# Kernel tuning notes

Measured on AMD Instinct MI355X. Metric: run time of the kernel, lower is better.

## Reference

```python
import jax, jax.numpy as jnp
import numpy as np

D_MODEL = 1024
N_HEADS = 16
HEAD_DIM = D_MODEL // N_HEADS
ROPE_THETA = 10000.0


def _rope_cache(seq_len, head_dim, dtype, theta=ROPE_THETA):
    half = head_dim // 2
    inv_freq = 1.0 / theta ** (jnp.arange(half, dtype=jnp.float32) / half)
    t = jnp.arange(seq_len, dtype=jnp.float32)
    freqs = jnp.outer(t, inv_freq)                 # [L, half]
    emb = jnp.concatenate([freqs, freqs], axis=-1)  # [L, head_dim]
    return jnp.cos(emb).astype(dtype), jnp.sin(emb).astype(dtype)


def _rotate_half(x):
    d = x.shape[-1]
    x1, x2 = x[..., : d // 2], x[..., d // 2 :]
    return jnp.concatenate([-x2, x1], axis=-1)


def _apply_rope(x, cos, sin):
    return x * cos + _rotate_half(x) * sin


def setup_inputs() -> dict:
    key = jax.random.key(0)
    ks = jax.random.split(key, 9)
    B, L, D = 2, 2048, D_MODEL
    s = 1.0 / np.sqrt(D)
    return {
        "x": jax.random.normal(ks[0], (B, L, D), dtype=jnp.float32),
        "Wq": jax.random.normal(ks[1], (D, D), dtype=jnp.float32) * s,
        "bq": jnp.zeros((D,), dtype=jnp.float32),
        "Wk": jax.random.normal(ks[2], (D, D), dtype=jnp.float32) * s,
        "bk": jnp.zeros((D,), dtype=jnp.float32),
        "Wv": jax.random.normal(ks[3], (D, D), dtype=jnp.float32) * s,
        "bv": jnp.zeros((D,), dtype=jnp.float32),
        "Wo": jax.random.normal(ks[4], (D, D), dtype=jnp.float32) * s,
        "bo": jnp.zeros((D,), dtype=jnp.float32),
    }


def reference(x, Wq, bq, Wk, bk, Wv, bv, Wo, bo):
    B, L, D = x.shape
    H, Hd = N_HEADS, HEAD_DIM
    scale = Hd ** -0.5

    def proj(W, b):
        # [B,L,D] -> [B,H,L,Hd]
        return (x @ W.T + b).reshape(B, L, H, Hd).transpose(0, 2, 1, 3)

    q = proj(Wq, bq)
    k = proj(Wk, bk)
    v = proj(Wv, bv)

    cos, sin = _rope_cache(L, Hd, x.dtype)  # [L, Hd]
    q = _apply_rope(q, cos, sin)
    k = _apply_rope(k, cos, sin)

    scores = jnp.einsum("bhqd,bhkd->bhqk", q, k) * scale  # [B,H,L,L]
    attn = jax.nn.softmax(scores, axis=-1)
    ctx = jnp.einsum("bhqk,bhkd->bhqd", attn, v)           # [B,H,L,Hd]
    ctx = ctx.transpose(0, 2, 1, 3).reshape(B, L, D)
    return ctx @ Wo.T + bo
```

## Files before the change

### kernel.cpp

```cpp
#include <hip/hip_runtime.h>

typedef unsigned short u16;
typedef unsigned int u32;
typedef __attribute__((ext_vector_type(8))) __bf16 bf16v8;
typedef __attribute__((ext_vector_type(4))) __bf16 bf16v4;
typedef __attribute__((ext_vector_type(4))) float f32x4;
typedef __attribute__((ext_vector_type(16))) float f32x16;
typedef __attribute__((ext_vector_type(2))) unsigned u32x2;

#define SEQ    2048
#define NBATCH 2
#define NHEAD  16
#define HD     64
#define DM     1024
#define MROWS  4096

__device__ __forceinline__ u16 f2bf(float f) {
  unsigned int u = __float_as_uint(f);
  u += 0x7FFFu + ((u >> 16) & 1u);
  return (u16)(u >> 16);
}

__device__ __forceinline__ void gll16(const void* g, void* l) {
  __builtin_amdgcn_global_load_lds(
      (__attribute__((address_space(1))) void*)g,
      (__attribute__((address_space(3))) void*)l, 16, 0, 0);
}

__global__ __launch_bounds__(256) void k_prep(
    const float* __restrict__ x,
    const float* __restrict__ Wq, const float* __restrict__ Wk,
    const float* __restrict__ Wv, const float* __restrict__ Wo,
    u16* __restrict__ Xb, u16* __restrict__ Wqb, u16* __restrict__ Wkb,
    u16* __restrict__ Wvb, u16* __restrict__ Wob,
    float* __restrict__ cosT, float* __restrict__ sinT) {
  int bid = blockIdx.x;
  if (bid < MROWS * DM / 1024) {
    int i = bid * 256 + threadIdx.x;
    float4 v = ((const float4*)x)[i];
    ushort4 o;
    o.x = f2bf(v.x); o.y = f2bf(v.y); o.z = f2bf(v.z); o.w = f2bf(v.w);
    ((ushort4*)Xb)[i] = o;
    return;
  }
  bid -= MROWS * DM / 1024;
  if (bid < 4 * (DM * DM / 1024)) {
    int seg = bid >> 10;
    int i = (bid & 1023) * 256 + threadIdx.x;
    const float* src = (seg == 0) ? Wq : (seg == 1) ? Wk : (seg == 2) ? Wv : Wo;
    u16* dst = (seg == 0) ? Wqb : (seg == 1) ? Wkb : (seg == 2) ? Wvb : Wob;
    float4 v = ((const float4*)src)[i];
    ushort4 o;
    o.x = f2bf(v.x); o.y = f2bf(v.y); o.z = f2bf(v.z); o.w = f2bf(v.w);
    ((ushort4*)dst)[i] = o;
    return;
  }
  bid -= 4 * (DM * DM / 1024);
  int idx = bid * 256 + threadIdx.x;
  int l = idx >> 5, d = idx & 31;
  float inv = 1.0f / powf(10000.0f, (float)d * (1.0f / 32.0f));
  float ang = (float)l * inv;
  float s, c;
  sincosf(ang, &s, &c);
  cosT[idx] = c;
  sinT[idx] = s;
}

__global__ __launch_bounds__(256) void k_gemm_qkv(
    const u16* __restrict__ A,
    const u16* W0, const u16* W1, const u16* W2,
    const float* b0, const float* b1, const float* b2,
    u16* __restrict__ Qr, u16* __restrict__ Kg, u16* __restrict__ Vg,
    const float* __restrict__ cosT, const float* __restrict__ sinT) {
  __shared__ __attribute__((aligned(16))) u16 As[64 * 64];
  __shared__ __attribute__((aligned(16))) u16 Bs[128 * 64];
  const int z = blockIdx.z;
  const u16* W = (z == 0) ? W0 : ((z == 1) ? W1 : W2);
  const float* bias = (z == 0) ? b0 : ((z == 1) ? b1 : b2);

  const int tid = threadIdx.x;
  const int lane = tid & 63, wid = tid >> 6;
  const int g = lane >> 4, c = lane & 15;
  const int wm = wid >> 1, wn = wid & 1;
  const int bm = blockIdx.x, bn = blockIdx.y;

  const f32x4 vz = {0.f, 0.f, 0.f, 0.f};
  f32x4 acc[2][4];
#pragma unroll
  for (int i = 0; i < 2; i++)
#pragma unroll
    for (int j = 0; j < 4; j++) acc[i][j] = vz;

  const int srow = tid >> 3;
  const int scb = tid & 7;

  for (int kt = 0; kt < DM / 64; ++kt) {
    __syncthreads();
#pragma unroll
    for (int cc = 0; cc < 2; ++cc) {
      int row = cc * 32 + srow;
      int sc = scb ^ (row & 7);
      gll16(A + (size_t)(bm * 64 + row) * DM + kt * 64 + sc * 8,
            &As[cc * 2048 + wid * 512]);
    }
#pragma unroll
    for (int cc = 0; cc < 4; ++cc) {
      int row = cc * 32 + srow;
      int sc = scb ^ (row & 7);
      gll16(W + (size_t)(bn * 128 + row) * DM + kt * 64 + sc * 8,
            &Bs[cc * 2048 + wid * 512]);
    }
    __syncthreads();
#pragma unroll
    for (int kk = 0; kk < 2; ++kk) {
      bf16v8 av[2], bv[4];
#pragma unroll
      for (int i = 0; i < 2; i++) {
        int row = wm * 32 + i * 16 + c;
        int sc = (kk * 4 + g) ^ (row & 7);
        av[i] = *(const bf16v8*)&As[row * 64 + sc * 8];
      }
#pragma unroll
      for (int j = 0; j < 4; j++) {
        int row = wn * 64 + j * 16 + c;
        int sc = (kk * 4 + g) ^ (row & 7);
        bv[j] = *(const bf16v8*)&Bs[row * 64 + sc * 8];
      }
#pragma unroll
      for (int i = 0; i < 2; i++)
#pragma unroll
        for (int j = 0; j < 4; j++)
          acc[i][j] = __builtin_amdgcn_mfma_f32_16x16x32_bf16(av[i], bv[j], acc[i][j], 0, 0, 0);
    }
  }

  if (z == 2) {
    const int h = bn * 2 + wn;
#pragma unroll
    for (int i = 0; i < 2; i++) {
      int m0 = bm * 64 + wm * 32 + i * 16 + g * 4;
#pragma unroll
      for (int r = 0; r < 4; r++) {
        int m = m0 + r;
        int tok = m & (SEQ - 1);
        int b = m >> 11;
        size_t base = ((size_t)((b * NHEAD + h) * 256 + (tok >> 3)) * 64) * 8 + (tok & 7);
#pragma unroll
        for (int j = 0; j < 4; j++) {
          int d = j * 16 + c;
          Vg[base + (size_t)d * 8] = f2bf(acc[i][j][r] + bias[bn * 128 + wn * 64 + d]);
        }
      }
    }
  } else if (z == 1) {
    const int h = bn * 2 + wn;
    const int nb = bn * 128 + wn * 64;
#pragma unroll
    for (int i = 0; i < 2; i++) {
      int m0 = bm * 64 + wm * 32 + i * 16 + g * 4;
#pragma unroll
      for (int r = 0; r < 4; r++) {
        int m = m0 + r;
        int tok = m & (SEQ - 1);
        int b = m >> 11;
        size_t bhb = (size_t)(b * NHEAD + h) * 8;
#pragma unroll
        for (int j = 0; j < 2; j++) {
          int d = j * 16 + c;
          float x1 = acc[i][j][r] + bias[nb + d];
          float x2 = acc[i][j + 2][r] + bias[nb + d + 32];
          float cs = cosT[tok * 32 + d];
          float sn = sinT[tok * 32 + d];
          Kg[(bhb + (d >> 3)) * (SEQ * 8) + tok * 8 + (d & 7)]     = f2bf(x1 * cs - x2 * sn);
          Kg[(bhb + 4 + (d >> 3)) * (SEQ * 8) + tok * 8 + (d & 7)] = f2bf(x2 * cs + x1 * sn);
        }
      }
    }
  } else {
    const float qs = 0.180336880f;
    const int h = bn * 2 + wn;
    const int nb = bn * 128 + wn * 64;
#pragma unroll
    for (int i = 0; i < 2; i++) {
      int m0 = bm * 64 + wm * 32 + i * 16 + g * 4;
#pragma unroll
      for (int r = 0; r < 4; r++) {
        int m = m0 + r;
        int tok = m & (SEQ - 1);
        int b = m >> 11;
        size_t obase = ((size_t)(b * NHEAD + h) * SEQ + tok) * HD;
#pragma unroll
        for (int j = 0; j < 2; j++) {
          int d = j * 16 + c;
          float x1 = acc[i][j][r] + bias[nb + d];
          float x2 = acc[i][j + 2][r] + bias[nb + d + 32];
          float cs = cosT[tok * 32 + d];
          float sn = sinT[tok * 32 + d];
          Qr[obase + d]      = f2bf((x1 * cs - x2 * sn) * qs);
          Qr[obase + d + 32] = f2bf((x2 * cs + x1 * sn) * qs);
        }
      }
    }
  }
}

__global__ __launch_bounds__(256) void k_gemm_out(
    const u16* __restrict__ A, const u16* __restrict__ W,
    const float* __restrict__ bias, float* __restrict__ out) {
  __shared__ __attribute__((aligned(16))) u16 As[128 * 64];
  __shared__ __attribute__((aligned(16))) u16 Bs[64 * 64];
  const int tid = threadIdx.x;
  const int lane = tid & 63, wid = tid >> 6;
  const int g = lane >> 4, c = lane & 15;
  const int wm = wid >> 1, wn = wid & 1;
  const int bm = blockIdx.x, bn = blockIdx.y;

  const f32x4 vz = {0.f, 0.f, 0.f, 0.f};
  f32x4 acc[4][2];
#pragma unroll
  for (int i = 0; i < 4; i++)
#pragma unroll
    for (int j = 0; j < 2; j++) acc[i][j] = vz;

  const int srow = tid >> 3;
  const int scb = tid & 7;

  for (int kt = 0; kt < DM / 64; ++kt) {
    __syncthreads();
#pragma unroll
    for (int cc = 0; cc < 4; ++cc) {
      int row = cc * 32 + srow;
      int sc = scb ^ (row & 7);
      gll16(A + (size_t)(bm * 128 + row) * DM + kt * 64 + sc * 8,
            &As[cc * 2048 + wid * 512]);
    }
#pragma unroll
    for (int cc = 0; cc < 2; ++cc) {
      int row = cc * 32 + srow;
      int sc = scb ^ (row & 7);
      gll16(W + (size_t)(bn * 64 + row) * DM + kt * 64 + sc * 8,
            &Bs[cc * 2048 + wid * 512]);
    }
    __syncthreads();
#pragma unroll
    for (int kk = 0; kk < 2; ++kk) {
      bf16v8 av[4], bv[2];
#pragma unroll
      for (int i = 0; i < 4; i++) {
        int row = wm * 64 + i * 16 + c;
        int sc = (kk * 4 + g) ^ (row & 7);
        av[i] = *(const bf16v8*)&As[row * 64 + sc * 8];
      }
#pragma unroll
      for (int j = 0; j < 2; j++) {
        int row = wn * 32 + j * 16 + c;
        int sc = (kk * 4 + g) ^ (row & 7);
        bv[j] = *(const bf16v8*)&Bs[row * 64 + sc * 8];
      }
#pragma unroll
      for (int i = 0; i < 4; i++)
#pragma unroll
        for (int j = 0; j < 2; j++)
          acc[i][j] = __builtin_amdgcn_mfma_f32_16x16x32_bf16(av[i], bv[j], acc[i][j], 0, 0, 0);
    }
  }

#pragma unroll
  for (int i = 0; i < 4; i++) {
    int m = bm * 128 + wm * 64 + i * 16 + g * 4;
#pragma unroll
    for (int j = 0; j < 2; j++) {
      int n = bn * 64 + wn * 32 + j * 16 + c;
      float bb = bias[n];
#pragma unroll
      for (int r = 0; r < 4; r++)
        out[(size_t)(m + r) * DM + n] = acc[i][j][r] + bb;
    }
  }
}

__global__ __launch_bounds__(512, 4) void k_attn(
    const u16* __restrict__ Qb, const u16* __restrict__ Kg,
    const u16* __restrict__ Vg, u16* __restrict__ Cb) {
  __shared__ __attribute__((aligned(16))) u16 SMEM[32768];
  const int tid = threadIdx.x, lane = tid & 63, wid = tid >> 6;
  const int hh = lane >> 5, ln = lane & 31;
  const int team = wid >> 2, lw = wid & 3;
  const int bh = blockIdx.y;
  const int q0 = blockIdx.x * 128 + lw * 32;

  const u16* Qh = Qb + ((size_t)bh * SEQ + q0 + ln) * HD + hh * 8;
  bf16v8 qf[4];
#pragma unroll
  for (int ks = 0; ks < 4; ks++) qf[ks] = *(const bf16v8*)(Qh + ks * 16);

  f32x16 octx[2];
#pragma unroll
  for (int dsub = 0; dsub < 2; dsub++)
#pragma unroll
    for (int r = 0; r < 16; r++) octx[dsub][r] = 0.f;
  f32x4 lac4 = {0.f, 0.f, 0.f, 0.f};

  const int kvbase = team * 1024;

#define STAGE(buf, kv0)                                                              \
  {                                                                                  \
    u16* Kb_ = &SMEM[(team * 2 + (buf)) * 8192];                                     \
    u16* Vb_ = Kb_ + 4096;                                                           \
    _Pragma("unroll") for (int cc = 0; cc < 2; ++cc) {                               \
      int kk = lw * 2 + cc;                                                          \
      gll16(Kg + ((size_t)(bh * 8 + kk) * SEQ + (kv0)) * 8 + lane * 8,               \
            &Kb_[kk * 512]);                                                         \
      gll16(Vg + ((size_t)(bh * 256 + ((kv0) >> 3) + kk) * 64 + lane) * 8,           \
            &Vb_[kk * 512]);                                                         \
    }                                                                                \
  }

  STAGE(0, kvbase);
  __syncthreads();
  int cur = 0;

  for (int it = 0; it < 16; ++it) {
    if (it + 1 < 16) STAGE(cur ^ 1, kvbase + (it + 1) * 64);
    const u16* Kc = &SMEM[(team * 2 + cur) * 8192];
    const u16* Vc = Kc + 4096;

    bf16v8 pb[4];
#pragma unroll
    for (int s = 0; s < 2; s++) {
      f32x16 sT;
#pragma unroll
      for (int r = 0; r < 16; r++) sT[r] = 0.f;
#pragma unroll
      for (int ks = 0; ks < 4; ks++) {
        bf16v8 kf = *(const bf16v8*)&Kc[(ks * 2 + hh) * 512 + (s * 32 + ln) * 8];
        sT = __builtin_amdgcn_mfma_f32_32x32x16_bf16(kf, qf[ks], sT, 0, 0, 0);
      }
      float p[16];
#pragma unroll
      for (int r = 0; r < 16; r++) {
        p[r] = __builtin_amdgcn_exp2f(sT[r]);
        lac4[r & 3] += p[r];
      }
#pragma unroll
      for (int ksl = 0; ksl < 2; ksl++) {
        const int bb = ksl * 8;
        u32 Aw, Bw, Cw, Dw;
        asm("v_cvt_pk_bf16_f32 %0, %1, %2" : "=v"(Aw) : "v"(p[bb + 0]), "v"(p[bb + 1]));
        asm("v_cvt_pk_bf16_f32 %0, %1, %2" : "=v"(Bw) : "v"(p[bb + 2]), "v"(p[bb + 3]));
        asm("v_cvt_pk_bf16_f32 %0, %1, %2" : "=v"(Cw) : "v"(p[bb + 4]), "v"(p[bb + 5]));
        asm("v_cvt_pk_bf16_f32 %0, %1, %2" : "=v"(Dw) : "v"(p[bb + 6]), "v"(p[bb + 7]));
        u32x2 r02 = __builtin_amdgcn_permlane32_swap(Aw, Cw, false, false);
        u32x2 r13 = __builtin_amdgcn_permlane32_swap(Bw, Dw, false, false);
        union { u32 w[4]; bf16v8 v; } pu;
        pu.w[0] = r02[0]; pu.w[1] = r13[0]; pu.w[2] = r02[1]; pu.w[3] = r13[1];
        pb[s * 2 + ksl] = pu.v;
      }
    }

#pragma unroll
    for (int dsub = 0; dsub < 2; dsub++)
#pragma unroll
      for (int ks = 0; ks < 4; ks++) {
        bf16v8 vf = *(const bf16v8*)&Vc[(ks * 2 + hh) * 512 + (dsub * 32 + ln) * 8];
        octx[dsub] = __builtin_amdgcn_mfma_f32_32x32x16_bf16(vf, pb[ks], octx[dsub], 0, 0, 0);
      }

    __syncthreads();
    cur ^= 1;
  }

  float lacc = (lac4[0] + lac4[1]) + (lac4[2] + lac4[3]);
  float lt_own = lacc + __shfl_xor(lacc, 32);

  float* Mo = (float*)SMEM;
  float* Ml = ((float*)SMEM) + 8192;
  __syncthreads();
  if (team == 1) {
#pragma unroll
    for (int dsub = 0; dsub < 2; dsub++)
#pragma unroll
      for (int rr = 0; rr < 4; rr++) {
        f32x4 v = {octx[dsub][rr * 4 + 0], octx[dsub][rr * 4 + 1],
                   octx[dsub][rr * 4 + 2], octx[dsub][rr * 4 + 3]};
        *(f32x4*)&Mo[(((lw * 8) + dsub * 4 + rr) * 64 + lane) * 4] = v;
      }
    if (hh == 0) Ml[lw * 32 + ln] = lt_own;
  }
  __syncthreads();
  if (team == 0) {
    float lt = lt_own + Ml[lw * 32 + ln];
    float inv = 1.0f / lt;
    const int b = bh >> 4, h = bh & 15;
    const int q = q0 + ln;
    u16* orow = Cb + ((size_t)(b * SEQ + q)) * DM + h * HD;
#pragma unroll
    for (int dsub = 0; dsub < 2; dsub++)
#pragma unroll
      for (int rr = 0; rr < 4; rr++) {
        f32x4 m = *(const f32x4*)&Mo[(((lw * 8) + dsub * 4 + rr) * 64 + lane) * 4];
        int d0 = dsub * 32 + rr * 8 + hh * 4;
        bf16v4 o4 = {(__bf16)((octx[dsub][rr * 4 + 0] + m[0]) * inv),
                     (__bf16)((octx[dsub][rr * 4 + 1] + m[1]) * inv),
                     (__bf16)((octx[dsub][rr * 4 + 2] + m[2]) * inv),
                     (__bf16)((octx[dsub][rr * 4 + 3] + m[3]) * inv)};
        *(bf16v4*)(orow + d0) = o4;
      }
  }
}

extern "C" void kernel_launch(void* const* d_in, const int* in_sizes, int n_in,
                              void* d_out, int out_size, void* d_ws, size_t ws_size,
                              hipStream_t stream) {
  (void)in_sizes; (void)n_in; (void)out_size;
  const float* x  = (const float*)d_in[0];
  const float* Wq = (const float*)d_in[1];
  const float* bq = (const float*)d_in[2];
  const float* Wk = (const float*)d_in[3];
  const float* bk = (const float*)d_in[4];
  const float* Wv = (const float*)d_in[5];
  const float* bv = (const float*)d_in[6];
  const float* Wo = (const float*)d_in[7];
  const float* bo = (const float*)d_in[8];
  float* out = (float*)d_out;
  char* ws = (char*)d_ws;
  const size_t MB = 1024ull * 1024ull;

  if (ws_size < 49ull * MB) return;

  float* cosT = (float*)(ws);
  float* sinT = (float*)(ws + 256 * 1024);
  u16* Xb  = (u16*)(ws + 512 * 1024);
  u16* Wqb = (u16*)(ws + 512 * 1024 + 8 * MB);
  u16* Wkb = (u16*)(ws + 512 * 1024 + 10 * MB);
  u16* Wvb = (u16*)(ws + 512 * 1024 + 12 * MB);
  u16* Wob = (u16*)(ws + 512 * 1024 + 14 * MB);
  u16* Qr  = (u16*)(ws + 512 * 1024 + 24 * MB);
  u16* Kg  = (u16*)(ws + 512 * 1024 + 32 * MB);
  u16* Vg  = (u16*)(ws + 512 * 1024 + 40 * MB);
  u16* Cb  = Xb;

  k_prep<<<dim3(8448), 256, 0, stream>>>(x, Wq, Wk, Wv, Wo, Xb, Wqb, Wkb, Wvb, Wob,
                                         cosT, sinT);

  dim3 gp(MROWS / 64, DM / 128, 3);
  k_gemm_qkv<<<gp, 256, 0, stream>>>(Xb, Wqb, Wkb, Wvb, bq, bk, bv, Qr, Kg, Vg,
                                     cosT, sinT);

  dim3 ga(SEQ / 128, NBATCH * NHEAD);
  k_attn<<<ga, 512, 0, stream>>>(Qr, Kg, Vg, Cb);

  dim3 go(MROWS / 128, DM / 64);
  k_gemm_out<<<go, 256, 0, stream>>>(Cb, Wob, bo, out);
}
```

Measured before the change: 104.8 us.

## Shrink out-proj tiles, remap attention grid, compute row sums via MFMA

After: 104.4 us, median of 2. About the same (-0.5%).

```diff
diff --git a/kernel.cpp b/kernel.cpp
--- a/kernel.cpp
+++ b/kernel.cpp
@@ -207,7 +207,7 @@
 __global__ __launch_bounds__(256) void k_gemm_out(
     const u16* __restrict__ A, const u16* __restrict__ W,
     const float* __restrict__ bias, float* __restrict__ out) {
-  __shared__ __attribute__((aligned(16))) u16 As[128 * 64];
+  __shared__ __attribute__((aligned(16))) u16 As[64 * 64];
   __shared__ __attribute__((aligned(16))) u16 Bs[64 * 64];
   const int tid = threadIdx.x;
   const int lane = tid & 63, wid = tid >> 6;
@@ -216,9 +216,9 @@
   const int bm = blockIdx.x, bn = blockIdx.y;
 
   const f32x4 vz = {0.f, 0.f, 0.f, 0.f};
-  f32x4 acc[4][2];
-#pragma unroll
-  for (int i = 0; i < 4; i++)
+  f32x4 acc[2][2];
+#pragma unroll
+  for (int i = 0; i < 2; i++)
 #pragma unroll
     for (int j = 0; j < 2; j++) acc[i][j] = vz;
 
@@ -227,27 +227,22 @@
 
   for (int kt = 0; kt < DM / 64; ++kt) {
     __syncthreads();
-#pragma unroll
-    for (int cc = 0; cc < 4; ++cc) {
-      int row = cc * 32 + srow;
-      int sc = scb ^ (row & 7);
-      gll16(A + (size_t)(bm * 128 + row) * DM + kt * 64 + sc * 8,
-            &As[cc * 2048 + wid * 512]);
-    }
 #pragma unroll
     for (int cc = 0; cc < 2; ++cc) {
       int row = cc * 32 + srow;
       int sc = scb ^ (row & 7);
+      gll16(A + (size_t)(bm * 64 + row) * DM + kt * 64 + sc * 8,
+            &As[cc * 2048 + wid * 512]);
       gll16(W + (size_t)(bn * 64 + row) * DM + kt * 64 + sc * 8,
             &Bs[cc * 2048 + wid * 512]);
     }
     __syncthreads();
 #pragma unroll
     for (int kk = 0; kk < 2; ++kk) {
-      bf16v8 av[4], bv[2];
-#pragma unroll
-      for (int i = 0; i < 4; i++) {
-        int row = wm * 64 + i * 16 + c;
+      bf16v8 av[2], bv[2];
+#pragma unroll
+      for (int i = 0; i < 2; i++) {
+        int row = wm * 32 + i * 16 + c;
         int sc = (kk * 4 + g) ^ (row & 7);
         av[i] = *(const bf16v8*)&As[row * 64 + sc * 8];
       }
@@ -258,7 +253,7 @@
         bv[j] = *(const bf16v8*)&Bs[row * 64 + sc * 8];
       }
 #pragma unroll
-      for (int i = 0; i < 4; i++)
+      for (int i = 0; i < 2; i++)
 #pragma unroll
         for (int j = 0; j < 2; j++)
           acc[i][j] = __builtin_amdgcn_mfma_f32_16x16x32_bf16(av[i], bv[j], acc[i][j], 0, 0, 0);
@@ -266,8 +261,8 @@
   }
 
 #pragma unroll
-  for (int i = 0; i < 4; i++) {
-    int m = bm * 128 + wm * 64 + i * 16 + g * 4;
+  for (int i = 0; i < 2; i++) {
+    int m = bm * 64 + wm * 32 + i * 16 + g * 4;
 #pragma unroll
     for (int j = 0; j < 2; j++) {
       int n = bn * 64 + wn * 32 + j * 16 + c;
@@ -286,20 +281,25 @@
   const int tid = threadIdx.x, lane = tid & 63, wid = tid >> 6;
   const int hh = lane >> 5, ln = lane & 31;
   const int team = wid >> 2, lw = wid & 3;
-  const int bh = blockIdx.y;
-  const int q0 = blockIdx.x * 128 + lw * 32;
+  const int id = blockIdx.x;
+  const int bh = (id & 7) * 4 + ((id >> 3) & 3);
+  const int q0 = (id >> 5) * 128 + lw * 32;
 
   const u16* Qh = Qb + ((size_t)bh * SEQ + q0 + ln) * HD + hh * 8;
   bf16v8 qf[4];
 #pragma unroll
   for (int ks = 0; ks < 4; ks++) qf[ks] = *(const bf16v8*)(Qh + ks * 16);
 
-  f32x16 octx[2];
+  const __bf16 one = (__bf16)1.0f;
+  const bf16v8 ones = {one, one, one, one, one, one, one, one};
+
+  f32x16 octx[2], lone;
 #pragma unroll
   for (int dsub = 0; dsub < 2; dsub++)
 #pragma unroll
     for (int r = 0; r < 16; r++) octx[dsub][r] = 0.f;
-  f32x4 lac4 = {0.f, 0.f, 0.f, 0.f};
+#pragma unroll
+  for (int r = 0; r < 16; r++) lone[r] = 0.f;
 
   const int kvbase = team * 1024;
 
@@ -331,17 +331,16 @@
       f32x16 sT;
 #pragma unroll
       for (int r = 0; r < 16; r++) sT[r] = 0.f;
+      __builtin_amdgcn_s_setprio(1);
 #pragma unroll
       for (int ks = 0; ks < 4; ks++) {
         bf16v8 kf = *(const bf16v8*)&Kc[(ks * 2 + hh) * 512 + (s * 32 + ln) * 8];
         sT = __builtin_amdgcn_mfma_f32_32x32x16_bf16(kf, qf[ks], sT, 0, 0, 0);
       }
+      __builtin_amdgcn_s_setprio(0);
       float p[16];
 #pragma unroll
-      for (int r = 0; r < 16; r++) {
-        p[r] = __builtin_amdgcn_exp2f(sT[r]);
-        lac4[r & 3] += p[r];
-      }
+      for (int r = 0; r < 16; r++) p[r] = __builtin_amdgcn_exp2f(sT[r]);
 #pragma unroll
       for (int ksl = 0; ksl < 2; ksl++) {
         const int bb = ksl * 8;
@@ -358,20 +357,23 @@
       }
     }
 
-#pragma unroll
-    for (int dsub = 0; dsub < 2; dsub++)
-#pragma unroll
-      for (int ks = 0; ks < 4; ks++) {
+    __builtin_amdgcn_s_setprio(1);
+#pragma unroll
+    for (int ks = 0; ks < 4; ks++) {
+      lone = __builtin_amdgcn_mfma_f32_32x32x16_bf16(ones, pb[ks], lone, 0, 0, 0);
+#pragma unroll
+      for (int dsub = 0; dsub < 2; dsub++) {
         bf16v8 vf = *(const bf16v8*)&Vc[(ks * 2 + hh) * 512 + (dsub * 32 + ln) * 8];
         octx[dsub] = __builtin_amdgcn_mfma_f32_32x32x16_bf16(vf, pb[ks], octx[dsub], 0, 0, 0);
       }
+    }
+    __builtin_amdgcn_s_setprio(0);
 
     __syncthreads();
     cur ^= 1;
   }
 
-  float lacc = (lac4[0] + lac4[1]) + (lac4[2] + lac4[3]);
-  float lt_own = lacc + __shfl_xor(lacc, 32);
+  float lt_own = lone[0];
 
   float* Mo = (float*)SMEM;
   float* Ml = ((float*)SMEM) + 8192;
@@ -447,9 +449,8 @@
   k_gemm_qkv<<<gp, 256, 0, stream>>>(Xb, Wqb, Wkb, Wvb, bq, bk, bv, Qr, Kg, Vg,
                                      cosT, sinT);
 
-  dim3 ga(SEQ / 128, NBATCH * NHEAD);
-  k_attn<<<ga, 512, 0, stream>>>(Qr, Kg, Vg, Cb);
-
-  dim3 go(MROWS / 128, DM / 64);
+  k_attn<<<dim3(SEQ / 128 * NBATCH * NHEAD), 512, 0, stream>>>(Qr, Kg, Vg, Cb);
+
+  dim3 go(MROWS / 64, DM / 64);
   k_gemm_out<<<go, 256, 0, stream>>>(Cb, Wob, bo, out);
 }
```
